# Optimization experiments

Hardware: AMD Instinct MI355X
Metric: run time of the kernel (lower is better)

Reference implementation:

```python
import jax, jax.numpy as jnp
import numpy as np

Q, B, D, NH, DH, DI, M = 1024, 4, 1024, 16, 64, 4096, 1024
K = Q + M  # klen
SCALE_W = 0.02
LN_EPS = 1e-5


def _layer_norm(x, g, b):
    mu = jnp.mean(x, axis=-1, keepdims=True)
    var = jnp.var(x, axis=-1, keepdims=True)
    return (x - mu) * jax.lax.rsqrt(var + LN_EPS) * g + b


def _rel_shift(x):
    # x: [qlen, klen, bsz, n_head] -> Transformer-XL relative shift
    q, k = x.shape[0], x.shape[1]
    zero_pad = jnp.zeros((q, 1) + x.shape[2:], x.dtype)
    x_padded = jnp.concatenate([zero_pad, x], axis=1)          # [q, k+1, b, n]
    x_padded = x_padded.reshape((k + 1, q) + x.shape[2:])      # [k+1, q, b, n]
    return x_padded[1:].reshape(x.shape)


def setup_inputs() -> dict:
    key = jax.random.key(0)
    ks = jax.random.split(key, 12)
    f32 = jnp.float32
    inp = {
        "w": jax.random.normal(ks[0], (Q, B, D), f32),
        "r": jax.random.normal(ks[1], (K, 1, D), f32),
        "mems": jax.random.normal(ks[2], (M, B, D), f32),
        "qkv_w": SCALE_W * jax.random.normal(ks[3], (D, 3 * NH * DH), f32),
        "r_net_w": SCALE_W * jax.random.normal(ks[4], (D, NH * DH), f32),
        "o_w": SCALE_W * jax.random.normal(ks[5], (NH * DH, D), f32),
        "r_w_bias": SCALE_W * jax.random.normal(ks[6], (NH, DH), f32),
        "r_r_bias": SCALE_W * jax.random.normal(ks[7], (NH, DH), f32),
        "ln1_g": jnp.ones((D,), f32),
        "ln1_b": jnp.zeros((D,), f32),
        "ff_w1": SCALE_W * jax.random.normal(ks[8], (D, DI), f32),
        "ff_b1": jnp.zeros((DI,), f32),
        "ff_w2": SCALE_W * jax.random.normal(ks[9], (DI, D), f32),
        "ff_b2": jnp.zeros((D,), f32),
        "ln2_g": jnp.ones((D,), f32),
        "ln2_b": jnp.zeros((D,), f32),
        # causal mask with memory: query i attends to keys j <= i + mem_len
        "attn_mask": jnp.arange(K)[None, :] > (jnp.arange(Q)[:, None] + M),
    }
    return inp


def reference(w, r, mems, qkv_w, r_net_w, o_w, r_w_bias, r_r_bias,
              ln1_g, ln1_b, ff_w1, ff_b1, ff_w2, ff_b2, ln2_g, ln2_b,
              attn_mask):
    qlen, bsz = w.shape[0], w.shape[1]
    # --- relative multi-head attention (post-lnorm, mems concat) ---
    cat = jnp.concatenate([mems, w], axis=0)                   # [klen, b, d]
    w_heads = cat @ qkv_w                                      # [klen, b, 3*nh*dh]
    r_head_k = (r @ r_net_w).reshape(-1, NH, DH)               # [rlen, nh, dh]
    q_h, k_h, v_h = jnp.split(w_heads, 3, axis=-1)
    klen = k_h.shape[0]
    q_h = q_h[-qlen:].reshape(qlen, bsz, NH, DH)
    k_h = k_h.reshape(klen, bsz, NH, DH)
    v_h = v_h.reshape(klen, bsz, NH, DH)

    rw_q = q_h + r_w_bias[None, None]                          # [q, b, nh, dh]
    AC = jnp.einsum('ibnd,jbnd->ijbn', rw_q, k_h)
    rr_q = q_h + r_r_bias[None, None]
    BD = jnp.einsum('ibnd,jnd->ijbn', rr_q, r_head_k)
    BD = _rel_shift(BD)

    scale = 1.0 / (DH ** 0.5)
    attn_score = (AC + BD) * scale                             # [q, k, b, nh]
    attn_score = jnp.where(attn_mask[:, :, None, None], -jnp.inf, attn_score)
    attn_prob = jax.nn.softmax(attn_score, axis=1)
    attn_vec = jnp.einsum('ijbn,jbnd->ibnd', attn_prob, v_h)
    attn_out = attn_vec.reshape(qlen, bsz, NH * DH) @ o_w      # [q, b, d]
    out = _layer_norm(w + attn_out, ln1_g, ln1_b)

    # --- position-wise FFN (post-lnorm) ---
    core = jax.nn.relu(out @ ff_w1 + ff_b1) @ ff_w2 + ff_b2
    out = _layer_norm(out + core, ln2_g, ln2_b)
    return out
```

## Files before the change

kernel.cpp:

```cpp
#include <hip/hip_runtime.h>
#include <math.h>


#define QLEN 1024
#define BSZ  4
#define DMODEL 1024
#define NHEAD 16
#define DHEAD 64
#define DINNER 4096
#define MEMLEN 1024
#define KLEN 2048

typedef __attribute__((ext_vector_type(8))) short short8;
typedef __attribute__((ext_vector_type(4))) short short4_t;
typedef __attribute__((ext_vector_type(4))) float f32x4;

__device__ __forceinline__ unsigned short f2bf(float x) {
  union { float f; unsigned u; } cv; cv.f = x;
  const unsigned u = cv.u;
  return (unsigned short)((u + 0x7FFFu + ((u >> 16) & 1u)) >> 16);
}
__device__ __forceinline__ float bf2f(unsigned short b) {
  union { unsigned u; float f; } cv; cv.u = ((unsigned)b) << 16;
  return cv.f;
}

__device__ __forceinline__ void gload16(const void* g, void* l) {
  __builtin_amdgcn_global_load_lds(
      (const __attribute__((address_space(1))) unsigned int*)g,
      (__attribute__((address_space(3))) unsigned int*)l, 16, 0, 0);
}

__device__ __forceinline__ int chidx(int row, int kc) {
  return row * 4 + (kc ^ ((row >> 1) & 3));
}

template<int MODE>
__global__ __launch_bounds__(512, 2) void mgemm2(
    const unsigned short* __restrict__ A, const unsigned short* __restrict__ Bt,
    unsigned short* __restrict__ Cb, const float* __restrict__ aux,
    unsigned short* __restrict__ oK, unsigned short* __restrict__ oV,
    int Kdim, int N)
{
  __shared__ __align__(16) char smem[65536];

  const int tid = threadIdx.x;
  const int lane = tid & 63, wv = tid >> 6;
  const int wr = wv >> 2, wc = wv & 3;
  const int quad = lane >> 4, l15 = lane & 15;

  const int gx = (int)gridDim.x;
  const int nwg = gx * (int)gridDim.y;
  const int flat = (int)blockIdx.y * gx + (int)blockIdx.x;
  const int swz = (flat & 7) * (nwg >> 3) + (flat >> 3);
  const int m0 = (swz / gx) * 256, n0 = (swz % gx) * 256;

  const int srow = tid >> 2;
  const int skc = (tid & 3) ^ ((srow >> 1) & 3);
  const unsigned short* pA0 = A + (size_t)(m0 + srow) * Kdim + skc * 8;
  const unsigned short* pA1 = A + (size_t)(m0 + 128 + srow) * Kdim + skc * 8;
  const unsigned short* pB0 = Bt + (size_t)(n0 + srow) * Kdim + skc * 8;
  const unsigned short* pB1 = Bt + (size_t)(n0 + 128 + srow) * Kdim + skc * 8;
  const int wb = (tid & 448) * 16;

  const int cch = (quad ^ ((l15 >> 1) & 3)) * 16;
  const int aoffb = wr * 8192 + l15 * 64 + cch;
  const int boffb = 32768 + (wc >> 1) * 8192 +
                    ((wc & 1) * 64 + l15) * 64 + cch;

  f32x4 acc[8][4] = {};

  const int nkt = Kdim >> 5;
  gload16(pA0, smem + wb);
  gload16(pA1, smem + 8192 + wb);
  gload16(pB0, smem + 32768 + wb);
  gload16(pB1, smem + 40960 + wb);
  pA0 += 32; pA1 += 32; pB0 += 32; pB1 += 32;

  for (int kt = 0; kt < nkt; ++kt) {
    const int bo = (kt & 1) * 16384;
    if (kt + 1 < nkt) {
      const int nb = bo ^ 16384;
      gload16(pA0, smem + nb + wb);
      gload16(pA1, smem + nb + 8192 + wb);
      gload16(pB0, smem + 32768 + nb + wb);
      gload16(pB1, smem + 40960 + nb + wb);
      pA0 += 32; pA1 += 32; pB0 += 32; pB1 += 32;
      asm volatile("s_waitcnt vmcnt(4)" ::: "memory");
    } else {
      asm volatile("s_waitcnt vmcnt(0)" ::: "memory");
    }
    __builtin_amdgcn_s_barrier();

    short8 bfr[4], af[4];
#pragma unroll
    for (int j = 0; j < 4; ++j)
      bfr[j] = *(const short8*)(smem + bo + boffb + j * 1024);
#pragma unroll
    for (int i = 0; i < 4; ++i)
      af[i] = *(const short8*)(smem + bo + aoffb + i * 1024);
    __builtin_amdgcn_s_setprio(1);
#pragma unroll
    for (int i = 0; i < 4; ++i)
#pragma unroll
      for (int j = 0; j < 4; ++j)
        acc[i][j] = __builtin_amdgcn_mfma_f32_16x16x32_bf16(
            af[i], bfr[j], acc[i][j], 0, 0, 0);
    __builtin_amdgcn_s_setprio(0);
    __builtin_amdgcn_s_barrier();

#pragma unroll
    for (int i = 0; i < 4; ++i)
      af[i] = *(const short8*)(smem + bo + aoffb + (i + 4) * 1024);
    __builtin_amdgcn_s_setprio(1);
#pragma unroll
    for (int i = 0; i < 4; ++i)
#pragma unroll
      for (int j = 0; j < 4; ++j)
        acc[i + 4][j] = __builtin_amdgcn_mfma_f32_16x16x32_bf16(
            af[i], bfr[j], acc[i + 4][j], 0, 0, 0);
    __builtin_amdgcn_s_setprio(0);
    __builtin_amdgcn_s_barrier();
  }

  const int rb0 = m0 + wr * 128 + quad * 4;
  const int cb0 = n0 + wc * 64 + l15;
#pragma unroll
  for (int i = 0; i < 8; ++i) {
#pragma unroll
    for (int r = 0; r < 4; ++r) {
      const int grow = rb0 + i * 16 + r;
#pragma unroll
      for (int j = 0; j < 4; ++j) {
        const int gcol = cb0 + j * 16;
        const float v = acc[i][j][r];
        if constexpr (MODE == 0) {
          const int kkg = grow >> 2, b2 = grow & 3;
          const int sec = gcol >> 10, hn = (gcol >> 6) & 15, d = gcol & 63;
          const unsigned short bv = f2bf(v);
          if (sec == 0) {
            if (kkg >= MEMLEN)
              Cb[((size_t)(b2 * NHEAD + hn) * QLEN + (kkg - MEMLEN)) * DHEAD + d] = bv;
          } else if (sec == 1) {
            oK[((size_t)(b2 * NHEAD + hn) * KLEN + kkg) * DHEAD + d] = bv;
          } else {
            oV[((size_t)(b2 * NHEAD + hn) * KLEN + kkg) * DHEAD + d] = bv;
          }
        } else {
          Cb[(size_t)grow * N + gcol] = f2bf(fmaxf(v + aux[gcol], 0.f));
        }
      }
    }
  }
}

template<int MODE, int TN>
__global__ __launch_bounds__(256) void mgemm(
    const unsigned short* __restrict__ A, const unsigned short* __restrict__ Bt,
    float* __restrict__ C, unsigned short* __restrict__ Cb,
    const float* __restrict__ aux, const float* __restrict__ res,
    int Kdim, int N)
{
  constexpr int BUF = 8192 + TN * 64;
  __shared__ __align__(16) char smem[2 * BUF];

  const int tid = threadIdx.x;
  const int lane = tid & 63, wv = tid >> 6;

  const int gx = (int)gridDim.x;
  const int nwg = gx * (int)gridDim.y;
  const int flat = (int)blockIdx.y * gx + (int)blockIdx.x;
  const int swz = (flat & 7) * (nwg >> 3) + (flat >> 3);
  const int m0 = (swz / gx) * 128, n0 = (swz % gx) * TN;

  const unsigned short *gA0, *gA1, *gB0;
  {
    int c = tid, m = c >> 2, kc = (c & 3) ^ ((m >> 1) & 3);
    gA0 = A + (size_t)(m0 + m) * Kdim + kc * 8;
    c = 256 + tid; m = c >> 2; kc = (c & 3) ^ ((m >> 1) & 3);
    gA1 = A + (size_t)(m0 + m) * Kdim + kc * 8;
    c = tid; int nn = c >> 2; kc = (c & 3) ^ ((nn >> 1) & 3);
    gB0 = Bt + (size_t)(n0 + nn) * Kdim + kc * 8;
  }
  const int wvoff = (tid & 192) * 16;

  const int fr = lane & 15, kq = lane >> 4;
  constexpr int NJ = TN / 32;
  int aoff[4], boff[NJ];
#pragma unroll
  for (int t = 0; t < 4; ++t) {
    const int ra = (wv & 1) * 64 + t * 16 + fr;
    aoff[t] = chidx(ra, kq) * 16;
  }
#pragma unroll
  for (int t = 0; t < NJ; ++t) {
    const int rb = (wv >> 1) * (TN / 2) + t * 16 + fr;
    boff[t] = 8192 + chidx(rb, kq) * 16;
  }

  f32x4 acc[4][NJ] = {};

  {
    char* const b0 = smem + wvoff;
    gload16(gA0, b0);
    gload16(gA1, b0 + 4096);
    gload16(gB0, b0 + 8192);
    gA0 += 32; gA1 += 32; gB0 += 32;
  }

  int cur = 0;
  for (int k0 = 0; k0 < Kdim; k0 += 32) {
    if (k0 + 32 < Kdim) {
      char* const nb = smem + (cur ^ 1) * BUF + wvoff;
      gload16(gA0, nb);
      gload16(gA1, nb + 4096);
      gload16(gB0, nb + 8192);
      gA0 += 32; gA1 += 32; gB0 += 32;
      asm volatile("s_waitcnt vmcnt(3)" ::: "memory");
    } else {
      asm volatile("s_waitcnt vmcnt(0)" ::: "memory");
    }
    __builtin_amdgcn_s_barrier();

    const char* const cb = smem + cur * BUF;
    short8 af[4], bfr[NJ];
#pragma unroll
    for (int t = 0; t < 4; ++t) af[t] = *(const short8*)(cb + aoff[t]);
#pragma unroll
    for (int t = 0; t < NJ; ++t) bfr[t] = *(const short8*)(cb + boff[t]);
#pragma unroll
    for (int i = 0; i < 4; ++i)
#pragma unroll
      for (int j = 0; j < NJ; ++j)
        acc[i][j] = __builtin_amdgcn_mfma_f32_16x16x32_bf16(
            af[i], bfr[j], acc[i][j], 0, 0, 0);

    asm volatile("s_waitcnt lgkmcnt(0)" ::: "memory");
    __builtin_amdgcn_s_barrier();
    cur ^= 1;
  }

  const int rbase = m0 + (wv & 1) * 64 + (lane >> 4) * 4;
  const int cbase = n0 + (wv >> 1) * (TN / 2) + (lane & 15);
#pragma unroll
  for (int i = 0; i < 4; ++i) {
#pragma unroll
    for (int r = 0; r < 4; ++r) {
      const int grow = rbase + i * 16 + r;
#pragma unroll
      for (int j = 0; j < NJ; ++j) {
        const int gcol = cbase + j * 16;
        const float v = acc[i][j][r];
        if constexpr (MODE == 1) {
          const int hn = gcol >> 6, d = gcol & 63;
          Cb[((size_t)hn * KLEN + grow) * DHEAD + d] = f2bf(v);
        } else if constexpr (MODE == 2) {
          C[(size_t)grow * N + gcol] = v + res[(size_t)grow * N + gcol];
        } else {
          C[(size_t)grow * N + gcol] = v + aux[gcol] + res[(size_t)grow * N + gcol];
        }
      }
    }
  }
}

__global__ __launch_bounds__(256) void transpose_v(
    const unsigned short* __restrict__ Vh, unsigned short* __restrict__ Vt)
{
  __shared__ unsigned short t[64 * 80];
  const int j0 = (int)blockIdx.x * 64;
  const int bn = (int)blockIdx.y;
  const int tid = threadIdx.x;
#pragma unroll
  for (int it = 0; it < 2; ++it) {
    const int f = it * 256 + tid;
    const int j = f >> 3, d8 = (f & 7) * 8;
    const short8 v = *(const short8*)(Vh + ((size_t)bn * KLEN + j0 + j) * DHEAD + d8);
    *(short8*)(t + j * 80 + d8) = v;
  }
  __syncthreads();
  const int d = tid >> 2, jseg = (tid & 3) * 16;
  short8 o0, o1;
#pragma unroll
  for (int e = 0; e < 8; ++e) o0[e] = (short)t[(jseg + e) * 80 + d];
#pragma unroll
  for (int e = 0; e < 8; ++e) o1[e] = (short)t[(jseg + 8 + e) * 80 + d];
  unsigned short* op = Vt + ((size_t)bn * DHEAD + d) * KLEN + j0 + jseg;
  *(short8*)op = o0;
  *(short8*)(op + 8) = o1;
}

__global__ __launch_bounds__(256) void cast_all(
    const float* __restrict__ mems, const float* __restrict__ w,
    const float* __restrict__ r, unsigned short* __restrict__ Xcat,
    unsigned short* __restrict__ Rb16)
{
  const size_t i = ((size_t)blockIdx.x * 256 + threadIdx.x) * 8;
  const float* src;
  unsigned short* dst;
  if (i < 4194304)       { src = mems + i;          dst = Xcat + i; }
  else if (i < 8388608)  { src = w + (i - 4194304); dst = Xcat + i; }
  else                   { src = r + (i - 8388608); dst = Rb16 + (i - 8388608); }
  const float4 x = *(const float4*)src;
  const float4 y = *(const float4*)(src + 4);
  short8 v;
  v[0] = (short)f2bf(x.x); v[1] = (short)f2bf(x.y);
  v[2] = (short)f2bf(x.z); v[3] = (short)f2bf(x.w);
  v[4] = (short)f2bf(y.x); v[5] = (short)f2bf(y.y);
  v[6] = (short)f2bf(y.z); v[7] = (short)f2bf(y.w);
  *(short8*)dst = v;
}

__global__ __launch_bounds__(256) void transpose_all(
    const float* __restrict__ qkv_w, const float* __restrict__ r_net_w,
    const float* __restrict__ o_w, const float* __restrict__ ff_w1,
    const float* __restrict__ ff_w2,
    unsigned short* __restrict__ Wqkv, unsigned short* __restrict__ Wr,
    unsigned short* __restrict__ Wo, unsigned short* __restrict__ W1,
    unsigned short* __restrict__ W2)
{
  const int bid = (int)blockIdx.x;
  const float* in; unsigned short* out; int R, C, xt, loc;
  if (bid < 768)        { in = qkv_w;   out = Wqkv; R = 1024; C = 3072; xt = 48; loc = bid; }
  else if (bid < 1024)  { in = r_net_w; out = Wr;   R = 1024; C = 1024; xt = 16; loc = bid - 768; }
  else if (bid < 1280)  { in = o_w;     out = Wo;   R = 1024; C = 1024; xt = 16; loc = bid - 1024; }
  else if (bid < 2304)  { in = ff_w1;   out = W1;   R = 1024; C = 4096; xt = 64; loc = bid - 1280; }
  else                  { in = ff_w2;   out = W2;   R = 4096; C = 1024; xt = 16; loc = bid - 2304; }
  const int c0 = (loc % xt) * 64, r0 = (loc / xt) * 64;

  __shared__ float t[64][65];
  const int tid = threadIdx.x;
  const int rr = tid >> 4, cc = (tid & 15) * 4;
#pragma unroll
  for (int it = 0; it < 4; ++it) {
    const int rw = rr + it * 16;
    const float4 v = *(const float4*)(in + (size_t)(r0 + rw) * C + c0 + cc);
    t[rw][cc] = v.x; t[rw][cc + 1] = v.y; t[rw][cc + 2] = v.z; t[rw][cc + 3] = v.w;
  }
  __syncthreads();
  const int oc = tid >> 2, ob = (tid & 3) * 16;
#pragma unroll
  for (int j4 = 0; j4 < 4; ++j4) {
    short4_t o;
#pragma unroll
    for (int j = 0; j < 4; ++j) o[j] = (short)f2bf(t[ob + j4 * 4 + j][oc]);
    *(short4_t*)(out + (size_t)(c0 + oc) * R + r0 + ob + j4 * 4) = o;
  }
}

__global__ __launch_bounds__(256, 2) void attn_mfma(
    const unsigned short* __restrict__ Qh, const unsigned short* __restrict__ Kh,
    const unsigned short* __restrict__ Vt, const unsigned short* __restrict__ Rk,
    const float* __restrict__ rwb, const float* __restrict__ rrb,
    float* __restrict__ Opart0, float* __restrict__ Opart1,
    float* __restrict__ den0, float* __restrict__ den1)
{
  __shared__ __align__(16) char smem[65536];

  const int tid = threadIdx.x;
  const int lane = tid & 63, wv = tid >> 6;
  const int quad = lane >> 4, l15 = lane & 15;

  const int bid0 = (int)blockIdx.y * 32 + (int)blockIdx.x;
  const int slot = bid0 >> 3;
  const int bn = (bid0 & 7) * 8 + (slot >> 5);
  const int inner = slot & 31;
  const int it = inner >> 1, sp = inner & 1;
  const int i0 = it * 64;
  const int n = bn & 15;

  const int nch = 17 + it;
  const int h = (nch + 1) >> 1;
  const int lo = sp ? h : 0, hi = sp ? nch : h;

  const unsigned short* __restrict__ Qb = Qh + (size_t)bn * QLEN * DHEAD;
  const unsigned short* __restrict__ Kb = Kh + (size_t)bn * KLEN * DHEAD;
  const unsigned short* __restrict__ Vb = Vt + (size_t)bn * DHEAD * KLEN;
  const unsigned short* __restrict__ Rb = Rk + (size_t)n * KLEN * DHEAD;

  short8 qk[2], qr[2];
  {
    const int qrow = i0 + wv * 16 + l15;
    const unsigned short* qp = Qb + (size_t)qrow * DHEAD + quad * 8;
    const float* wp = rwb + n * DHEAD + quad * 8;
    const float* rp = rrb + n * DHEAD + quad * 8;
#pragma unroll
    for (int ks = 0; ks < 2; ++ks) {
      const short8 q8 = *(const short8*)(qp + ks * 32);
#pragma unroll
      for (int e = 0; e < 8; ++e) {
        const float qv = bf2f((unsigned short)q8[e]);
        qk[ks][e] = (short)f2bf(qv + wp[ks * 32 + e]);
        qr[ks][e] = (short)f2bf(qv + rp[ks * 32 + e]);
      }
    }
  }

  int srcl[4];
  bool condE[4];
#pragma unroll
  for (int r = 0; r < 4; ++r) {
    const int E = l15 - quad * 4 - r + 15;
    srcl[r] = (lane & 48) | (E & 15);
    condE[r] = (E >= 16);
  }

  f32x4 O[4] = {};
  float rden[4] = {0.f, 0.f, 0.f, 0.f};
  const int wvoff = (tid & 192) * 16;

  {
    const int j0 = lo * 64;
    const int g64 = lo - it + 15;
    const int rb3 = (g64 % 3) * 64;
#pragma unroll
    for (int t2 = 0; t2 < 2; ++t2) {
      const int s = t2 * 256 + tid;
      const int row = s >> 3, kc = (s & 7) ^ (row & 7);
      gload16(Kb + (((size_t)(j0 + row)) << 6) + kc * 8,
              smem + t2 * 4096 + wvoff);
    }
#pragma unroll
    for (int t2 = 0; t2 < 2; ++t2) {
      const int s = t2 * 256 + tid;
      const int row = s >> 3, kc = (s & 7) ^ (row & 7);
      gload16(Vb + (((size_t)row) << 11) + j0 + kc * 8,
              smem + 16384 + t2 * 4096 + wvoff);
    }
    const int gw = j0 - i0 + 960;
#pragma unroll
    for (int t2 = 0; t2 < 4; ++t2) {
      const int rr = t2 * 32 + (tid >> 3);
      const int gr = gw + rr;
      const int kc = (tid & 7) ^ (rr & 7);
      int pb = rb3 + t2 * 32; if (pb >= 192) pb -= 192;
      gload16(Rb + (((size_t)gr) << 6) + kc * 8,
              smem + 32768 + pb * 128 + wvoff);
    }
  }

  int cur = 0;
  for (int ch = lo; ch < hi; ++ch) {
    const int j0 = ch * 64;
    const int g64 = ch - it + 15;
    const int rb3 = (g64 % 3) * 64;
    const int gw = j0 - i0 + 960;

    asm volatile("s_waitcnt lgkmcnt(0)" ::: "memory");
    __builtin_amdgcn_s_barrier();

    if (ch + 1 < hi) {
      const int nb = cur ^ 1;
      const int j0n = j0 + 64;
#pragma unroll
      for (int t2 = 0; t2 < 2; ++t2) {
        const int s = t2 * 256 + tid;
        const int row = s >> 3, kc = (s & 7) ^ (row & 7);
        gload16(Kb + (((size_t)(j0n + row)) << 6) + kc * 8,
                smem + nb * 8192 + t2 * 4096 + wvoff);
      }
#pragma unroll
      for (int t2 = 0; t2 < 2; ++t2) {
        const int s = t2 * 256 + tid;
        const int row = s >> 3, kc = (s & 7) ^ (row & 7);
        gload16(Vb + (((size_t)row) << 11) + j0n + kc * 8,
                smem + 16384 + nb * 8192 + t2 * 4096 + wvoff);
      }
#pragma unroll
      for (int t2 = 0; t2 < 2; ++t2) {
        const int rr = t2 * 32 + (tid >> 3);
        const int gr = gw + 128 + rr;
        const int kc = (tid & 7) ^ (rr & 7);
        int pb = rb3 + 128 + t2 * 32; if (pb >= 192) pb -= 192;
        gload16(Rb + (((size_t)gr) << 6) + kc * 8,
                smem + 32768 + pb * 128 + wvoff);
      }
      asm volatile("s_waitcnt vmcnt(6)" ::: "memory");
    } else {
      asm volatile("s_waitcnt vmcnt(0)" ::: "memory");
    }
    __builtin_amdgcn_s_barrier();

    const char* const kbase = smem + cur * 8192;
    const char* const vbase = smem + 16384 + cur * 8192;

    f32x4 sk[4];
#pragma unroll
    for (int jt = 0; jt < 4; ++jt) {
      f32x4 a = {0.f, 0.f, 0.f, 0.f};
#pragma unroll
      for (int ks = 0; ks < 2; ++ks) {
        const int frr = jt * 16 + l15;
        const int c = (ks * 4 + quad) ^ (l15 & 7);
        const short8 kf = *(const short8*)(kbase + (frr * 8 + c) * 16);
        a = __builtin_amdgcn_mfma_f32_16x16x32_bf16(qk[ks], kf, a, 0, 0, 0);
      }
      sk[jt] = a;
    }
    f32x4 uu[5];
#pragma unroll
    for (int s = 0; s < 5; ++s) {
      f32x4 a = {0.f, 0.f, 0.f, 0.f};
      int frr = rb3 + (3 - wv + s) * 16 + l15;
      if (frr >= 192) frr -= 192;
#pragma unroll
      for (int ks = 0; ks < 2; ++ks) {
        const int c = (ks * 4 + quad) ^ (l15 & 7);
        const short8 rf = *(const short8*)(smem + 32768 + (frr * 8 + c) * 16);
        a = __builtin_amdgcn_mfma_f32_16x16x32_bf16(qr[ks], rf, a, 0, 0, 0);
      }
      uu[s] = a;
    }

    float rot[5][4];
#pragma unroll
    for (int s = 0; s < 5; ++s)
#pragma unroll
      for (int r = 0; r < 4; ++r)
        rot[s][r] = __shfl(uu[s][r], srcl[r], 64);

    unsigned short* const Ps = (unsigned short*)(smem + 57344);
#pragma unroll
    for (int jt = 0; jt < 4; ++jt) {
      const int jl = jt * 16 + l15;
#pragma unroll
      for (int r = 0; r < 4; ++r) {
        const int il = wv * 16 + quad * 4 + r;
        const int dj = (j0 + jl) - (i0 + il);
        const float uv = condE[r] ? rot[jt + 1][r] : rot[jt][r];
        const float sv = (sk[jt][r] + uv) * 0.125f;
        const float p = (dj <= 1024) ? __expf(sv) : 0.f;
        rden[r] += p;
        Ps[(il * 8 + ((jl >> 3) ^ (il & 7))) * 8 + (jl & 7)] = f2bf(p);
      }
    }

#pragma unroll
    for (int ks = 0; ks < 2; ++ks) {
      const int frp = wv * 16 + l15;
      const int cp = (ks * 4 + quad) ^ (l15 & 7);
      const short8 pf = *(const short8*)(smem + 57344 + (frp * 8 + cp) * 16);
#pragma unroll
      for (int dt = 0; dt < 4; ++dt) {
        const int vr = dt * 16 + l15;
        const short8 vf = *(const short8*)(vbase + (vr * 8 + cp) * 16);
        O[dt] = __builtin_amdgcn_mfma_f32_16x16x32_bf16(pf, vf, O[dt], 0, 0, 0);
      }
    }
    cur ^= 1;
  }

#pragma unroll
  for (int m = 1; m < 16; m <<= 1)
#pragma unroll
    for (int r = 0; r < 4; ++r)
      rden[r] += __shfl_xor(rden[r], m, 64);

  float* const Op = sp ? Opart1 : Opart0;
  float* const dp = sp ? den1 : den0;
  const size_t ob = (size_t)(bn * 16 + it) * 64;
#pragma unroll
  for (int r = 0; r < 4; ++r) {
    const int il = wv * 16 + quad * 4 + r;
#pragma unroll
    for (int dt = 0; dt < 4; ++dt)
      Op[(ob + il) * 64 + dt * 16 + l15] = O[dt][r];
    if (l15 == 0) dp[ob + il] = rden[r];
  }
}

__global__ __launch_bounds__(256) void attn_combine(
    const float* __restrict__ O0, const float* __restrict__ O1,
    const float* __restrict__ d0, const float* __restrict__ d1,
    unsigned short* __restrict__ AVb)
{
  const int blk = (int)blockIdx.x;
  const int bn = blk >> 4, it = blk & 15;
  const int b = bn >> 4, n = bn & 15;
  const int tid = threadIdx.x;
  const int il = tid >> 2, ds = (tid & 3) * 16;
  const size_t base = ((size_t)blk * 64 + il) * 64 + ds;
  const float inv = 1.f / (d0[blk * 64 + il] + d1[blk * 64 + il]);
  short8 o0, o1;
#pragma unroll
  for (int g = 0; g < 2; ++g) {
    const float4 a = *(const float4*)(O0 + base + g * 8);
    const float4 bb = *(const float4*)(O1 + base + g * 8);
    const float4 a2 = *(const float4*)(O0 + base + g * 8 + 4);
    const float4 b2 = *(const float4*)(O1 + base + g * 8 + 4);
    short8& o = g ? o1 : o0;
    o[0] = (short)f2bf((a.x + bb.x) * inv);  o[1] = (short)f2bf((a.y + bb.y) * inv);
    o[2] = (short)f2bf((a.z + bb.z) * inv);  o[3] = (short)f2bf((a.w + bb.w) * inv);
    o[4] = (short)f2bf((a2.x + b2.x) * inv); o[5] = (short)f2bf((a2.y + b2.y) * inv);
    o[6] = (short)f2bf((a2.z + b2.z) * inv); o[7] = (short)f2bf((a2.w + b2.w) * inv);
  }
  unsigned short* op =
      AVb + ((size_t)(it * 64 + il) * BSZ + b) * DMODEL + n * DHEAD + ds;
  *(short8*)op = o0;
  *(short8*)(op + 8) = o1;
}

__global__ __launch_bounds__(256) void ln_kernel(
    float* __restrict__ X, const float* __restrict__ gw,
    const float* __restrict__ bw, unsigned short* __restrict__ bfo)
{
  const int row = blockIdx.x, tid = threadIdx.x;
  float* rp = X + (size_t)row * DMODEL;
  const float4 x = *(const float4*)(rp + tid * 4);
  float s = x.x + x.y + x.z + x.w;
  float q = x.x * x.x + x.y * x.y + x.z * x.z + x.w * x.w;
#pragma unroll
  for (int m = 1; m < 64; m <<= 1) {
    s += __shfl_xor(s, m, 64);
    q += __shfl_xor(q, m, 64);
  }
  __shared__ float ss[4], sq[4];
  if ((tid & 63) == 0) { ss[tid >> 6] = s; sq[tid >> 6] = q; }
  __syncthreads();
  s = ss[0] + ss[1] + ss[2] + ss[3];
  q = sq[0] + sq[1] + sq[2] + sq[3];
  const float mu = s * (1.f / DMODEL);
  const float var = q * (1.f / DMODEL) - mu * mu;
  const float rstd = rsqrtf(var + 1e-5f);
  const float4 g4 = *(const float4*)(gw + tid * 4);
  const float4 b4 = *(const float4*)(bw + tid * 4);
  float4 y;
  y.x = (x.x - mu) * rstd * g4.x + b4.x;
  y.y = (x.y - mu) * rstd * g4.y + b4.y;
  y.z = (x.z - mu) * rstd * g4.z + b4.z;
  y.w = (x.w - mu) * rstd * g4.w + b4.w;
  *(float4*)(rp + tid * 4) = y;
  if (bfo) {
    short4_t o;
    o[0] = (short)f2bf(y.x); o[1] = (short)f2bf(y.y);
    o[2] = (short)f2bf(y.z); o[3] = (short)f2bf(y.w);
    *(short4_t*)(bfo + (size_t)row * DMODEL + tid * 4) = o;
  }
}

extern "C" void kernel_launch(void* const* d_in, const int* in_sizes, int n_in,
                              void* d_out, int out_size, void* d_ws,
                              size_t ws_size, hipStream_t stream)
{
  const float* w       = (const float*)d_in[0];
  const float* r       = (const float*)d_in[1];
  const float* mems    = (const float*)d_in[2];
  const float* qkv_w   = (const float*)d_in[3];
  const float* r_net_w = (const float*)d_in[4];
  const float* o_w     = (const float*)d_in[5];
  const float* r_w_bias= (const float*)d_in[6];
  const float* r_r_bias= (const float*)d_in[7];
  const float* ln1_g   = (const float*)d_in[8];
  const float* ln1_b   = (const float*)d_in[9];
  const float* ff_w1   = (const float*)d_in[10];
  const float* ff_b1   = (const float*)d_in[11];
  const float* ff_w2   = (const float*)d_in[12];
  const float* ff_b2   = (const float*)d_in[13];
  const float* ln2_g   = (const float*)d_in[14];
  const float* ln2_b   = (const float*)d_in[15];
  float* out = (float*)d_out;

  float* X1 = (float*)d_ws;
  unsigned short* Qh   = (unsigned short*)(X1 + 4194304);
  unsigned short* Kh   = Qh + 4194304;
  unsigned short* Vt   = Kh + 8388608;
  unsigned short* Rk   = Vt + 8388608;
  unsigned short* Xcat = Rk + 2097152 + 8192;
  unsigned short* Wqkv = Xcat + 8388608;
  unsigned short* Wr   = Wqkv + 3145728;
  unsigned short* Wo   = Wr + 1048576;
  unsigned short* W1   = Wo + 1048576;
  unsigned short* W2   = W1 + 4194304;
  float* den0 = (float*)(W2 + 4194304);
  float* den1 = den0 + 65536;
  unsigned short* AVb  = (unsigned short*)(den1 + 65536);
  unsigned short* Vh     = (unsigned short*)X1;
  unsigned short* Rb16   = AVb;
  float* Opart0          = (float*)X1;
  float* Opart1          = (float*)Xcat;
  unsigned short* X1b    = Qh;
  unsigned short* H      = Kh;

  const dim3 blk(256);
  const dim3 blk2(512);

  cast_all<<<dim3(5120), blk, 0, stream>>>(mems, w, r, Xcat, Rb16);
  transpose_all<<<dim3(3328), blk, 0, stream>>>(
      qkv_w, r_net_w, o_w, ff_w1, ff_w2, Wqkv, Wr, Wo, W1, W2);

  mgemm2<0><<<dim3(12, 32), blk2, 0, stream>>>(
      Xcat, Wqkv, Qh, nullptr, Kh, Vh, DMODEL, 3 * DMODEL);
  transpose_v<<<dim3(32, 64), blk, 0, stream>>>(Vh, Vt);
  mgemm<1, 64><<<dim3(16, 16), blk, 0, stream>>>(
      Rb16, Wr, nullptr, Rk, nullptr, nullptr, DMODEL, DMODEL);
  attn_mfma<<<dim3(32, 64), blk, 0, stream>>>(
      Qh, Kh, Vt, Rk, r_w_bias, r_r_bias, Opart0, Opart1, den0, den1);
  attn_combine<<<dim3(1024), blk, 0, stream>>>(Opart0, Opart1, den0, den1, AVb);
  mgemm<2, 64><<<dim3(16, 32), blk, 0, stream>>>(
      AVb, Wo, X1, nullptr, nullptr, w, DMODEL, DMODEL);
  ln_kernel<<<dim3(4096), blk, 0, stream>>>(X1, ln1_g, ln1_b, X1b);
  mgemm2<3><<<dim3(16, 16), blk2, 0, stream>>>(
      X1b, W1, H, ff_b1, nullptr, nullptr, DMODEL, DINNER);
  mgemm<4, 64><<<dim3(16, 32), blk, 0, stream>>>(
      H, W2, out, nullptr, ff_b2, X1, DINNER, DMODEL);
  ln_kernel<<<dim3(4096), blk, 0, stream>>>(out, ln2_g, ln2_b, nullptr);

  (void)in_sizes; (void)n_in; (void)out_size; (void)ws_size;
}
```

Before: 519.4 us.

## Triple-buffer LDS in both bf16 GEMM kernels to prefetch two K-tiles ahead

Both MFMA GEMM kernels move from double to triple buffering of their shared-memory tiles. Global-to-LDS loads now run two K-steps ahead, with vmcnt waits adjusted to match, so more memory latency is hidden behind the matrix math. The large kernel's LDS grows to 96KB and drops its 2-blocks-per-CU launch bound, which may reduce occupancy. An explicit lgkmcnt wait is added before the end-of-iteration barrier.

```diff
diff --git a/kernel.cpp b/kernel.cpp
--- a/kernel.cpp
+++ b/kernel.cpp
@@ -36,13 +36,13 @@
 }
 
 template<int MODE>
-__global__ __launch_bounds__(512, 2) void mgemm2(
+__global__ __launch_bounds__(512) void mgemm2(
     const unsigned short* __restrict__ A, const unsigned short* __restrict__ Bt,
     unsigned short* __restrict__ Cb, const float* __restrict__ aux,
     unsigned short* __restrict__ oK, unsigned short* __restrict__ oV,
     int Kdim, int N)
 {
-  __shared__ __align__(16) char smem[65536];
+  __shared__ __align__(16) char smem[98304];
 
   const int tid = threadIdx.x;
   const int lane = tid & 63, wv = tid >> 6;
@@ -65,40 +65,50 @@
 
   const int cch = (quad ^ ((l15 >> 1) & 3)) * 16;
   const int aoffb = wr * 8192 + l15 * 64 + cch;
-  const int boffb = 32768 + (wc >> 1) * 8192 +
-                    ((wc & 1) * 64 + l15) * 64 + cch;
+  const int boffb = (wc >> 1) * 8192 + ((wc & 1) * 64 + l15) * 64 + cch;
 
   f32x4 acc[8][4] = {};
 
   const int nkt = Kdim >> 5;
   gload16(pA0, smem + wb);
   gload16(pA1, smem + 8192 + wb);
-  gload16(pB0, smem + 32768 + wb);
-  gload16(pB1, smem + 40960 + wb);
+  gload16(pB0, smem + 49152 + wb);
+  gload16(pB1, smem + 57344 + wb);
   pA0 += 32; pA1 += 32; pB0 += 32; pB1 += 32;
-
+  gload16(pA0, smem + 16384 + wb);
+  gload16(pA1, smem + 24576 + wb);
+  gload16(pB0, smem + 65536 + wb);
+  gload16(pB1, smem + 73728 + wb);
+  pA0 += 32; pA1 += 32; pB0 += 32; pB1 += 32;
+
+  int rbuf = 0;
   for (int kt = 0; kt < nkt; ++kt) {
-    const int bo = (kt & 1) * 16384;
-    if (kt + 1 < nkt) {
-      const int nb = bo ^ 16384;
-      gload16(pA0, smem + nb + wb);
-      gload16(pA1, smem + nb + 8192 + wb);
-      gload16(pB0, smem + 32768 + nb + wb);
-      gload16(pB1, smem + 40960 + nb + wb);
+    if (kt + 2 < nkt) {
+      int wb3 = rbuf + 2; if (wb3 >= 3) wb3 -= 3;
+      const int ab = wb3 * 16384, bb = 49152 + wb3 * 16384;
+      gload16(pA0, smem + ab + wb);
+      gload16(pA1, smem + ab + 8192 + wb);
+      gload16(pB0, smem + bb + wb);
+      gload16(pB1, smem + bb + 8192 + wb);
       pA0 += 32; pA1 += 32; pB0 += 32; pB1 += 32;
+      asm volatile("s_waitcnt vmcnt(8)" ::: "memory");
+    } else if (kt + 1 < nkt) {
       asm volatile("s_waitcnt vmcnt(4)" ::: "memory");
     } else {
       asm volatile("s_waitcnt vmcnt(0)" ::: "memory");
     }
     __builtin_amdgcn_s_barrier();
 
+    const char* const abuf = smem + rbuf * 16384;
+    const char* const bbuf = smem + 49152 + rbuf * 16384;
+
     short8 bfr[4], af[4];
 #pragma unroll
     for (int j = 0; j < 4; ++j)
-      bfr[j] = *(const short8*)(smem + bo + boffb + j * 1024);
+      bfr[j] = *(const short8*)(bbuf + boffb + j * 1024);
 #pragma unroll
     for (int i = 0; i < 4; ++i)
-      af[i] = *(const short8*)(smem + bo + aoffb + i * 1024);
+      af[i] = *(const short8*)(abuf + aoffb + i * 1024);
     __builtin_amdgcn_s_setprio(1);
 #pragma unroll
     for (int i = 0; i < 4; ++i)
@@ -111,7 +121,7 @@
 
 #pragma unroll
     for (int i = 0; i < 4; ++i)
-      af[i] = *(const short8*)(smem + bo + aoffb + (i + 4) * 1024);
+      af[i] = *(const short8*)(abuf + aoffb + (i + 4) * 1024);
     __builtin_amdgcn_s_setprio(1);
 #pragma unroll
     for (int i = 0; i < 4; ++i)
@@ -120,7 +130,9 @@
         acc[i + 4][j] = __builtin_amdgcn_mfma_f32_16x16x32_bf16(
             af[i], bfr[j], acc[i + 4][j], 0, 0, 0);
     __builtin_amdgcn_s_setprio(0);
+    asm volatile("s_waitcnt lgkmcnt(0)" ::: "memory");
     __builtin_amdgcn_s_barrier();
+    rbuf += 1; if (rbuf == 3) rbuf = 0;
   }
 
   const int rb0 = m0 + wr * 128 + quad * 4;
@@ -162,7 +174,7 @@
     int Kdim, int N)
 {
   constexpr int BUF = 8192 + TN * 64;
-  __shared__ __align__(16) char smem[2 * BUF];
+  __shared__ __align__(16) char smem[3 * BUF];
 
   const int tid = threadIdx.x;
   const int lane = tid & 63, wv = tid >> 6;
@@ -206,23 +218,31 @@
     gload16(gA1, b0 + 4096);
     gload16(gB0, b0 + 8192);
     gA0 += 32; gA1 += 32; gB0 += 32;
-  }
-
-  int cur = 0;
+    char* const b1 = smem + BUF + wvoff;
+    gload16(gA0, b1);
+    gload16(gA1, b1 + 4096);
+    gload16(gB0, b1 + 8192);
+    gA0 += 32; gA1 += 32; gB0 += 32;
+  }
+
+  int rbuf = 0;
   for (int k0 = 0; k0 < Kdim; k0 += 32) {
-    if (k0 + 32 < Kdim) {
-      char* const nb = smem + (cur ^ 1) * BUF + wvoff;
+    if (k0 + 64 < Kdim) {
+      int wb3 = rbuf + 2; if (wb3 >= 3) wb3 -= 3;
+      char* const nb = smem + wb3 * BUF + wvoff;
       gload16(gA0, nb);
       gload16(gA1, nb + 4096);
       gload16(gB0, nb + 8192);
       gA0 += 32; gA1 += 32; gB0 += 32;
+      asm volatile("s_waitcnt vmcnt(6)" ::: "memory");
+    } else if (k0 + 32 < Kdim) {
       asm volatile("s_waitcnt vmcnt(3)" ::: "memory");
     } else {
       asm volatile("s_waitcnt vmcnt(0)" ::: "memory");
     }
     __builtin_amdgcn_s_barrier();
 
-    const char* const cb = smem + cur * BUF;
+    const char* const cb = smem + rbuf * BUF;
     short8 af[4], bfr[NJ];
 #pragma unroll
     for (int t = 0; t < 4; ++t) af[t] = *(const short8*)(cb + aoff[t]);
@@ -237,7 +257,7 @@
 
     asm volatile("s_waitcnt lgkmcnt(0)" ::: "memory");
     __builtin_amdgcn_s_barrier();
-    cur ^= 1;
+    rbuf += 1; if (rbuf == 3) rbuf = 0;
   }
 
   const int rbase = m0 + (wv & 1) * 64 + (lane >> 4) * 4;
```

Result: no change. 521.2 us (+0.4%).
